# Performance work log

Hardware: AMD Instinct MI355X
Metric: run time of the kernel (lower is better)

Reference implementation:

```python
import jax, jax.numpy as jnp
import numpy as np

B, IN, H, OUT, T = 8192, 7, 256, 3, 200  # batch, input feats, hidden, output, seq_length


def setup_inputs() -> dict:
    key = jax.random.key(0)
    ks = iter(jax.random.split(key, 32))

    def W(shape, fan_in):
        return jax.random.normal(next(ks), shape, dtype=jnp.float32) * np.float32(1.0 / np.sqrt(fan_in))

    inp = {
        "x": jax.random.normal(next(ks), (B, IN), dtype=jnp.float32),
        # encoder: Linear(7,256) ReLU Linear(256,256) ReLU Linear(256,256) ReLU
        "enc_w1": W((H, IN), IN), "enc_b1": jnp.zeros((H,), jnp.float32),
        "enc_w2": W((H, H), H), "enc_b2": jnp.zeros((H,), jnp.float32),
        "enc_w3": W((H, H), H), "enc_b3": jnp.zeros((H,), jnp.float32),
        # hidden/cell init: Linear(256, 256*2)
        "hinit_w": W((2 * H, H), H), "hinit_b": jnp.zeros((2 * H,), jnp.float32),
        "cinit_w": W((2 * H, H), H), "cinit_b": jnp.zeros((2 * H,), jnp.float32),
        # LSTM layer 0 (input=3) and layer 1 (input=256); PyTorch gate order i,f,g,o
        "w_ih0": W((4 * H, OUT), H), "w_hh0": W((4 * H, H), H),
        "b_ih0": jnp.zeros((4 * H,), jnp.float32), "b_hh0": jnp.zeros((4 * H,), jnp.float32),
        "w_ih1": W((4 * H, H), H), "w_hh1": W((4 * H, H), H),
        "b_ih1": jnp.zeros((4 * H,), jnp.float32), "b_hh1": jnp.zeros((4 * H,), jnp.float32),
        # output head: Linear(256,128) ReLU Linear(128,3)
        "out_w1": W((H // 2, H), H), "out_b1": jnp.zeros((H // 2,), jnp.float32),
        "out_w2": W((OUT, H // 2), H // 2), "out_b2": jnp.zeros((OUT,), jnp.float32),
        "start_token": jnp.zeros((OUT,), jnp.float32),
    }
    return inp


def _lstm_cell(inp, h, c, w_ih, w_hh, b_ih, b_hh):
    gates = inp @ w_ih.T + b_ih + h @ w_hh.T + b_hh  # [B, 4H]
    i, f, g, o = jnp.split(gates, 4, axis=-1)
    c_new = jax.nn.sigmoid(f) * c + jax.nn.sigmoid(i) * jnp.tanh(g)
    h_new = jax.nn.sigmoid(o) * jnp.tanh(c_new)
    return h_new, c_new


def reference(x, enc_w1, enc_b1, enc_w2, enc_b2, enc_w3, enc_b3,
              hinit_w, hinit_b, cinit_w, cinit_b,
              w_ih0, w_hh0, b_ih0, b_hh0, w_ih1, w_hh1, b_ih1, b_hh1,
              out_w1, out_b1, out_w2, out_b2, start_token):
    b = x.shape[0]
    # MLP encoder (dropout inactive at inference)
    e = jax.nn.relu(x @ enc_w1.T + enc_b1)
    e = jax.nn.relu(e @ enc_w2.T + enc_b2)
    e = jax.nn.relu(e @ enc_w3.T + enc_b3)
    h0_all = (e @ hinit_w.T + hinit_b).reshape(b, 2, H)  # (batch, layers, H)
    c0_all = (e @ cinit_w.T + cinit_b).reshape(b, 2, H)
    h0, h1 = h0_all[:, 0], h0_all[:, 1]
    c0, c1 = c0_all[:, 0], c0_all[:, 1]
    dec = jnp.broadcast_to(start_token[None, :], (b, OUT))

    def step(carry, _):
        dec, h0, c0, h1, c1 = carry
        h0n, c0n = _lstm_cell(dec, h0, c0, w_ih0, w_hh0, b_ih0, b_hh0)
        h1n, c1n = _lstm_cell(h0n, h1, c1, w_ih1, w_hh1, b_ih1, b_hh1)
        out = jax.nn.relu(h1n @ out_w1.T + out_b1) @ out_w2.T + out_b2  # [B, 3]
        return (out, h0n, c0n, h1n, c1n), out

    _, outs = jax.lax.scan(step, (dec, h0, c0, h1, c1), None, length=T)
    return jnp.transpose(outs, (1, 0, 2))  # (batch, T, 3)
```

## Files before the change

### kernel.cpp

```cpp
#include <hip/hip_runtime.h>

typedef _Float16 f16;
typedef f16 h8v __attribute__((ext_vector_type(8)));
typedef f16 h4v __attribute__((ext_vector_type(4)));
typedef float f4v __attribute__((ext_vector_type(4)));

#define TT 200
#define NTHR 512
#define NWG 256

#define W0F   0
#define W1IF  262144
#define W1HF  524288
#define OW1F  786432
#define EW2F  819200
#define EW3F  884736
#define HIWF  950272
#define CIWF  1081344
#define FRAG_TOTAL 1212416
#define H0F   1212416
#define H1F   5406720
#define O1F   9601024
#define DECF  10649600
#define FLGF  10780672

#define FE1 0
#define FE2 1
#define FE3 2
#define FDEC 3
#define FH0 4
#define FH1 5
#define FO1 6

static __device__ __forceinline__ f4v mfma16(h8v a, h8v b, f4v c) {
  return __builtin_amdgcn_mfma_f32_16x16x32_f16(a, b, c, 0, 0, 0);
}
static __device__ __forceinline__ f4v fzero() { f4v z; z[0]=0.f; z[1]=0.f; z[2]=0.f; z[3]=0.f; return z; }
static __device__ __forceinline__ float rcpf(float x) { return __builtin_amdgcn_rcpf(x); }
static __device__ __forceinline__ float sigm(float x) { return rcpf(1.0f + __expf(-x)); }
static __device__ __forceinline__ float tanh2(float x) { return 1.0f - 2.0f * rcpf(1.0f + __expf(2.0f * x)); }

__global__ void conv_w(const float* __restrict__ whh0, const float* __restrict__ wih1,
                       const float* __restrict__ whh1, const float* __restrict__ ow1,
                       const float* __restrict__ ew2,  const float* __restrict__ ew3,
                       const float* __restrict__ hiw,  const float* __restrict__ ciw,
                       f16* __restrict__ dst, int* __restrict__ flags) {
  int i = blockIdx.x * 256 + threadIdx.x;
  if (blockIdx.x == 0 && threadIdx.x < 128) flags[threadIdx.x] = 0;
  if (i >= FRAG_TOTAL) return;
  const float* src; int base;
  if      (i < 262144)  { src = whh0; base = 0; }
  else if (i < 524288)  { src = wih1; base = 262144; }
  else if (i < 786432)  { src = whh1; base = 524288; }
  else if (i < 819200)  { src = ow1;  base = 786432; }
  else if (i < 884736)  { src = ew2;  base = 819200; }
  else if (i < 950272)  { src = ew3;  base = 884736; }
  else if (i < 1081344) { src = hiw;  base = 950272; }
  else                  { src = ciw;  base = 1081344; }
  int e = i - base;
  int row = e >> 8, col = e & 255;
  int idx = base + ((((row >> 4) << 5) + (col >> 3)) << 7) + ((row & 15) << 3) + (col & 7);
  dst[idx] = (f16)src[e];
}

#define RELF(fi)                                                               \
  do { __syncthreads();                                                        \
       if (tid == 0) __hip_atomic_fetch_add(&flg[fi], 1, __ATOMIC_RELAXED,     \
                                            __HIP_MEMORY_SCOPE_SYSTEM);        \
  } while (0)
#define WAITF(fi, tgt)                                                         \
  do { if (tid == 0) {                                                         \
         while (__hip_atomic_load(&flg[fi], __ATOMIC_RELAXED,                  \
                                  __HIP_MEMORY_SCOPE_SYSTEM) < (tgt))          \
           __builtin_amdgcn_s_sleep(2);                                        \
         (void)__hip_atomic_load(&flg[fi], __ATOMIC_ACQUIRE,                   \
                                 __HIP_MEMORY_SCOPE_SYSTEM);                   \
       }                                                                       \
       __syncthreads();                                                        \
  } while (0)

__global__ __launch_bounds__(NTHR, 1)
void traj_kernel(const float* __restrict__ x,
                 const float* __restrict__ ew1, const float* __restrict__ eb1,
                 const float* __restrict__ eb2, const float* __restrict__ eb3,
                 const float* __restrict__ hib, const float* __restrict__ cib,
                 const float* __restrict__ wih0,
                 const float* __restrict__ bih0, const float* __restrict__ bhh0,
                 const float* __restrict__ bih1, const float* __restrict__ bhh1,
                 const float* __restrict__ ob1, const float* __restrict__ ow2,
                 const float* __restrict__ ob2, const float* __restrict__ stok,
                 f16* __restrict__ ws, int* __restrict__ flags,
                 float* __restrict__ out)
{
  __shared__ __align__(16) f16 WL[13 * 4096];
  __shared__ __align__(16) float decsL[512 * 4];
  __shared__ __align__(16) f16 o1s[32 * 136];
  __shared__ float w2s[384];
  __shared__ float b0L[64];
  __shared__ float b1L[64];
  __shared__ float wiL[192];
  __shared__ float ob2s[4];

  const int tid  = threadIdx.x;
  const int bid  = blockIdx.x;
  const int g    = (bid & 7) + ((bid >> 7) << 3);
  const int m    = (bid >> 3) & 15;
  const int wv   = tid >> 6;
  const int lane = tid & 63;
  const int lr   = lane & 15;
  const int lg   = lane >> 4;

  int* flg = flags + g * 8;
  const int dcol = 16 * m + lr;

  f16* e1g = ws + H0F + g * 131072;
  f16* e2g = ws + H1F + g * 131072;
  f16* e3g = ws + H0F + (16 + g) * 131072;
  f16* o1g = ws + O1F + g * 65536;
  float* decb = (float*)(ws + DECF) + g * 4096;

  if (tid < 64) {
    const int G = tid >> 4, l = tid & 15;
    const int gc = G * 256 + 16 * m + l;
    b0L[tid] = bih0[gc] + bhh0[gc];
    b1L[tid] = bih1[gc] + bhh1[gc];
    wiL[tid * 3 + 0] = wih0[gc * 3 + 0];
    wiL[tid * 3 + 1] = wih0[gc * 3 + 1];
    wiL[tid * 3 + 2] = wih0[gc * 3 + 2];
  }
  const float ob1r = ob1[((m & 7) << 4) + lr];
  if (tid < 384) w2s[tid] = ow2[tid];
  if (tid < 3)   ob2s[tid] = ob2[tid];

  auto cptile = [&](int slot, int srcF) {
    ((h8v*)(WL + slot * 4096))[tid] = *(const h8v*)(ws + srcF + tid * 8);
  };
  auto BF = [&](int slot, int k) -> h8v {
    return ((const h8v*)WL)[slot * 512 + ((k << 2) + lg) * 16 + lr];
  };
  auto loadA8 = [&](const f16* gb, int R0, h8v* a) {
    const f16* p0 = gb + (lg >> 1) * 8192 + (size_t)(R0 + lr) * 16 + (lg & 1) * 8;
#pragma unroll
    for (int k = 0; k < 8; ++k) a[k] = *(const h8v*)(p0 + k * 16384);
  };

  cptile(0, EW2F + m * 4096);
  cptile(1, EW3F + m * 4096);
  cptile(2, HIWF + m * 4096);
  cptile(3, HIWF + (16 + m) * 4096);
  cptile(4, CIWF + m * 4096);
  cptile(5, CIWF + (16 + m) * 4096);
  __syncthreads();

  {
    const int r = tid;
    float xr[7];
#pragma unroll
    for (int k = 0; k < 7; ++k) xr[k] = x[(size_t)(g * 512 + r) * 7 + k];
    f16 ev[16];
#pragma unroll
    for (int i2 = 0; i2 < 16; ++i2) {
      const int c = 16 * m + i2;
      float a = eb1[c];
#pragma unroll
      for (int k = 0; k < 7; ++k) a += xr[k] * ew1[c * 7 + k];
      ev[i2] = (f16)fmaxf(a, 0.0f);
    }
    *(h8v*)(e1g + m * 8192 + r * 16)     = *(h8v*)&ev[0];
    *(h8v*)(e1g + m * 8192 + r * 16 + 8) = *(h8v*)&ev[8];
  }
  RELF(FE1); WAITF(FE1, 16);

  {
    const float bb = eb2[dcol];
#pragma unroll
    for (int mt = 0; mt < 4; ++mt) {
      const int R0 = wv * 64 + mt * 16;
      h8v a[8]; loadA8(e1g, R0, a);
      f4v acc = fzero();
#pragma unroll
      for (int k = 0; k < 8; ++k) acc = mfma16(a[k], BF(0, k), acc);
#pragma unroll
      for (int j = 0; j < 4; ++j)
        e2g[m * 8192 + (R0 + 4 * lg + j) * 16 + lr] = (f16)fmaxf(acc[j] + bb, 0.0f);
    }
  }
  RELF(FE2); WAITF(FE2, 16);

  {
    const float bb = eb3[dcol];
#pragma unroll
    for (int mt = 0; mt < 4; ++mt) {
      const int R0 = wv * 64 + mt * 16;
      h8v a[8]; loadA8(e2g, R0, a);
      f4v acc = fzero();
#pragma unroll
      for (int k = 0; k < 8; ++k) acc = mfma16(a[k], BF(1, k), acc);
#pragma unroll
      for (int j = 0; j < 4; ++j)
        e3g[m * 8192 + (R0 + 4 * lg + j) * 16 + lr] = (f16)fmaxf(acc[j] + bb, 0.0f);
    }
  }
  RELF(FE3); WAITF(FE3, 16);

  float c0v[4][4], c1v[4][4];
  {
    f16* h0g0 = ws + H0F + g * 131072;
    f16* h1g0 = ws + H1F + g * 131072;
    const float bh0 = hib[dcol], bh1 = hib[256 + dcol];
    const float bc0 = cib[dcol], bc1 = cib[256 + dcol];
#pragma unroll
    for (int mt = 0; mt < 4; ++mt) {
      const int R0 = wv * 64 + mt * 16;
      h8v a[8]; loadA8(e3g, R0, a);
      f4v aH = fzero(), aC = fzero();
#pragma unroll
      for (int k = 0; k < 8; ++k) { aH = mfma16(a[k], BF(2, k), aH); aC = mfma16(a[k], BF(4, k), aC); }
#pragma unroll
      for (int j = 0; j < 4; ++j) {
        h0g0[m * 8192 + (R0 + 4 * lg + j) * 16 + lr] = (f16)(aH[j] + bh0);
        c0v[mt][j] = aC[j] + bc0;
      }
      aH = fzero(); aC = fzero();
#pragma unroll
      for (int k = 0; k < 8; ++k) { aH = mfma16(a[k], BF(3, k), aH); aC = mfma16(a[k], BF(5, k), aC); }
#pragma unroll
      for (int j = 0; j < 4; ++j) {
        h1g0[m * 8192 + (R0 + 4 * lg + j) * 16 + lr] = (f16)(aH[j] + bh1);
        c1v[mt][j] = aC[j] + bc1;
      }
    }
    if (tid < 32) {
      f4v d; d[0] = stok[0]; d[1] = stok[1]; d[2] = stok[2]; d[3] = 0.f;
      *(f4v*)(decb + (m * 32 + tid) * 4) = d;
    }
  }
  RELF(FDEC);

#pragma unroll
  for (int G = 0; G < 4; ++G) {
    cptile(G,     W0F  + (G * 16 + m) * 4096);
    cptile(4 + G, W1IF + (G * 16 + m) * 4096);
    cptile(8 + G, W1HF + (G * 16 + m) * 4096);
  }
  cptile(12, OW1F + (m & 7) * 4096);
  __syncthreads();

  f4v g0a[4][4];
  WAITF(FDEC, 16);
  {
    const f16* h0old0 = ws + H0F + g * 131072;
#pragma unroll
    for (int mt = 0; mt < 4; ++mt) {
      const int R0 = wv * 64 + mt * 16;
      h8v a[8]; loadA8(h0old0, R0, a);
#pragma unroll
      for (int G = 0; G < 4; ++G) g0a[mt][G] = fzero();
#pragma unroll
      for (int k = 0; k < 8; ++k) {
        g0a[mt][0] = mfma16(a[k], BF(0, k), g0a[mt][0]);
        g0a[mt][1] = mfma16(a[k], BF(1, k), g0a[mt][1]);
        g0a[mt][2] = mfma16(a[k], BF(2, k), g0a[mt][2]);
        g0a[mt][3] = mfma16(a[k], BF(3, k), g0a[mt][3]);
      }
    }
  }

#pragma unroll 1
  for (int t = 0; t < TT; ++t) {
    const int p = t & 1;
    f16* h0new = ws + H0F + ((p ^ 1) * 16 + g) * 131072;
    f16* h1old = ws + H1F + (p * 16 + g) * 131072;
    f16* h1new = ws + H1F + ((p ^ 1) * 16 + g) * 131072;
    const float* decp = decb + p * 2048;
    float* decn = decb + (p ^ 1) * 2048;

    WAITF(FDEC, 16 * (t + 1));
    *(f4v*)(decsL + tid * 4) = *(const f4v*)(decp + tid * 4);
    __syncthreads();

    {
      float cb0[4], cw[4][3];
#pragma unroll
      for (int G = 0; G < 4; ++G) {
        cb0[G]   = b0L[G * 16 + lr];
        cw[G][0] = wiL[(G * 16 + lr) * 3 + 0];
        cw[G][1] = wiL[(G * 16 + lr) * 3 + 1];
        cw[G][2] = wiL[(G * 16 + lr) * 3 + 2];
      }
#pragma unroll
      for (int mt = 0; mt < 4; ++mt) {
        const int R0 = wv * 64 + mt * 16;
#pragma unroll
        for (int j = 0; j < 4; ++j) {
          const int row = R0 + 4 * lg + j;
          f4v d4 = *(const f4v*)(decsL + row * 4);
          float gi = g0a[mt][0][j] + cb0[0] + d4[0]*cw[0][0] + d4[1]*cw[0][1] + d4[2]*cw[0][2];
          float gf = g0a[mt][1][j] + cb0[1] + d4[0]*cw[1][0] + d4[1]*cw[1][1] + d4[2]*cw[1][2];
          float gg = g0a[mt][2][j] + cb0[2] + d4[0]*cw[2][0] + d4[1]*cw[2][1] + d4[2]*cw[2][2];
          float go = g0a[mt][3][j] + cb0[3] + d4[0]*cw[3][0] + d4[1]*cw[3][1] + d4[2]*cw[3][2];
          float cn = sigm(gf) * c0v[mt][j] + sigm(gi) * tanh2(gg);
          c0v[mt][j] = cn;
          h0new[m * 8192 + row * 16 + lr] = (f16)(sigm(go) * tanh2(cn));
        }
      }
    }
    RELF(FH0);

    f4v ph[2][4];
#pragma unroll
    for (int mt = 0; mt < 2; ++mt) {
      const int R0 = wv * 64 + mt * 16;
      h8v a[8]; loadA8(h1old, R0, a);
#pragma unroll
      for (int G = 0; G < 4; ++G) ph[mt][G] = fzero();
#pragma unroll
      for (int k = 0; k < 8; ++k) {
        ph[mt][0] = mfma16(a[k], BF(8,  k), ph[mt][0]);
        ph[mt][1] = mfma16(a[k], BF(9,  k), ph[mt][1]);
        ph[mt][2] = mfma16(a[k], BF(10, k), ph[mt][2]);
        ph[mt][3] = mfma16(a[k], BF(11, k), ph[mt][3]);
      }
    }
    WAITF(FH0, 16 * (t + 1));

    {
      float cb1[4];
#pragma unroll
      for (int G = 0; G < 4; ++G) cb1[G] = b1L[G * 16 + lr];
#pragma unroll
      for (int mt = 0; mt < 2; ++mt) {
        const int R0 = wv * 64 + mt * 16;
        h8v a[8]; loadA8(h0new, R0, a);
#pragma unroll
        for (int k = 0; k < 8; ++k) {
          ph[mt][0] = mfma16(a[k], BF(4, k), ph[mt][0]);
          ph[mt][1] = mfma16(a[k], BF(5, k), ph[mt][1]);
          ph[mt][2] = mfma16(a[k], BF(6, k), ph[mt][2]);
          ph[mt][3] = mfma16(a[k], BF(7, k), ph[mt][3]);
        }
#pragma unroll
        for (int j = 0; j < 4; ++j) {
          const int row = R0 + 4 * lg + j;
          float cn = sigm(ph[mt][1][j] + cb1[1]) * c1v[mt][j]
                   + sigm(ph[mt][0][j] + cb1[0]) * tanh2(ph[mt][2][j] + cb1[2]);
          c1v[mt][j] = cn;
          h1new[m * 8192 + row * 16 + lr] = (f16)(sigm(ph[mt][3][j] + cb1[3]) * tanh2(cn));
        }
      }
#pragma unroll
      for (int mt = 2; mt < 4; ++mt) {
        const int R0 = wv * 64 + mt * 16;
        f4v ai = fzero(), af = fzero(), ag = fzero(), ao = fzero();
        {
          h8v a[8]; loadA8(h1old, R0, a);
#pragma unroll
          for (int k = 0; k < 8; ++k) {
            ai = mfma16(a[k], BF(8,  k), ai);
            af = mfma16(a[k], BF(9,  k), af);
            ag = mfma16(a[k], BF(10, k), ag);
            ao = mfma16(a[k], BF(11, k), ao);
          }
        }
        {
          h8v a[8]; loadA8(h0new, R0, a);
#pragma unroll
          for (int k = 0; k < 8; ++k) {
            ai = mfma16(a[k], BF(4, k), ai);
            af = mfma16(a[k], BF(5, k), af);
            ag = mfma16(a[k], BF(6, k), ag);
            ao = mfma16(a[k], BF(7, k), ao);
          }
        }
#pragma unroll
        for (int j = 0; j < 4; ++j) {
          const int row = R0 + 4 * lg + j;
          float cn = sigm(af[j] + cb1[1]) * c1v[mt][j]
                   + sigm(ai[j] + cb1[0]) * tanh2(ag[j] + cb1[2]);
          c1v[mt][j] = cn;
          h1new[m * 8192 + row * 16 + lr] = (f16)(sigm(ao[j] + cb1[3]) * tanh2(cn));
        }
      }
    }
    RELF(FH1);

#pragma unroll
    for (int mt = 0; mt < 2; ++mt) {
      const int R0 = wv * 64 + mt * 16;
      h8v a[8]; loadA8(h0new, R0, a);
#pragma unroll
      for (int G = 0; G < 4; ++G) g0a[mt][G] = fzero();
#pragma unroll
      for (int k = 0; k < 8; ++k) {
        g0a[mt][0] = mfma16(a[k], BF(0, k), g0a[mt][0]);
        g0a[mt][1] = mfma16(a[k], BF(1, k), g0a[mt][1]);
        g0a[mt][2] = mfma16(a[k], BF(2, k), g0a[mt][2]);
        g0a[mt][3] = mfma16(a[k], BF(3, k), g0a[mt][3]);
      }
    }
    WAITF(FH1, 16 * (t + 1));

    {
      const int Rh = ((m >> 3) << 8) + wv * 32;
#pragma unroll
      for (int mt2 = 0; mt2 < 2; ++mt2) {
        const int R0 = Rh + mt2 * 16;
        h8v a[8]; loadA8(h1new, R0, a);
        f4v acc = fzero();
#pragma unroll
        for (int k = 0; k < 8; ++k) acc = mfma16(a[k], BF(12, k), acc);
#pragma unroll
        for (int j = 0; j < 4; ++j)
          o1g[(m & 7) * 8192 + (R0 + 4 * lg + j) * 16 + lr] =
              (f16)fmaxf(acc[j] + ob1r, 0.0f);
      }
    }
    RELF(FO1);

    {
      const int R0 = wv * 64 + 2 * 16;
      h8v a[8]; loadA8(h0new, R0, a);
#pragma unroll
      for (int G = 0; G < 4; ++G) g0a[2][G] = fzero();
#pragma unroll
      for (int k = 0; k < 8; ++k) {
        g0a[2][0] = mfma16(a[k], BF(0, k), g0a[2][0]);
        g0a[2][1] = mfma16(a[k], BF(1, k), g0a[2][1]);
        g0a[2][2] = mfma16(a[k], BF(2, k), g0a[2][2]);
        g0a[2][3] = mfma16(a[k], BF(3, k), g0a[2][3]);
      }
    }
    WAITF(FO1, 16 * (t + 1));

    {
      const int r32 = tid >> 4, t8 = (tid & 15) >> 1, hf = tid & 1;
      *(h8v*)(o1s + r32 * 136 + t8 * 16 + hf * 8) =
          *(const h8v*)(o1g + t8 * 8192 + (m * 32 + r32) * 16 + hf * 8);
    }
    __syncthreads();
    {
      const int r = tid >> 4, jj = tid & 15;
      float a0 = 0.f, a1 = 0.f, a2 = 0.f;
#pragma unroll
      for (int kk = 0; kk < 8; ++kk) {
        const int k = jj * 8 + kk;
        const float ov = (float)o1s[r * 136 + k];
        a0 += ov * w2s[k];
        a1 += ov * w2s[128 + k];
        a2 += ov * w2s[256 + k];
      }
#pragma unroll
      for (int s = 8; s >= 1; s >>= 1) {
        a0 += __shfl_xor(a0, s);
        a1 += __shfl_xor(a1, s);
        a2 += __shfl_xor(a2, s);
      }
      if (jj == 0) {
        a0 += ob2s[0]; a1 += ob2s[1]; a2 += ob2s[2];
        float* op = out + ((size_t)(g * 512 + m * 32 + r) * TT + t) * 3;
        op[0] = a0; op[1] = a1; op[2] = a2;
        f4v d; d[0] = a0; d[1] = a1; d[2] = a2; d[3] = 0.f;
        *(f4v*)(decn + (m * 32 + r) * 4) = d;
      }
    }
    RELF(FDEC);

    {
      const int R0 = wv * 64 + 3 * 16;
      h8v a[8]; loadA8(h0new, R0, a);
#pragma unroll
      for (int G = 0; G < 4; ++G) g0a[3][G] = fzero();
#pragma unroll
      for (int k = 0; k < 8; ++k) {
        g0a[3][0] = mfma16(a[k], BF(0, k), g0a[3][0]);
        g0a[3][1] = mfma16(a[k], BF(1, k), g0a[3][1]);
        g0a[3][2] = mfma16(a[k], BF(2, k), g0a[3][2]);
        g0a[3][3] = mfma16(a[k], BF(3, k), g0a[3][3]);
      }
    }
  }
}

extern "C" void kernel_launch(void* const* d_in, const int* in_sizes, int n_in,
                              void* d_out, int out_size, void* d_ws, size_t ws_size,
                              hipStream_t stream) {
  (void)in_sizes; (void)n_in; (void)out_size; (void)ws_size;
  f16* wk = (f16*)d_ws;
  int* flags = (int*)((char*)d_ws + (size_t)FLGF * 2);
  conv_w<<<(FRAG_TOTAL + 255) / 256, 256, 0, stream>>>(
      (const float*)d_in[12], (const float*)d_in[15],
      (const float*)d_in[16], (const float*)d_in[19],
      (const float*)d_in[3],  (const float*)d_in[5],
      (const float*)d_in[7],  (const float*)d_in[9],
      wk, flags);
  traj_kernel<<<NWG, NTHR, 0, stream>>>(
      (const float*)d_in[0],
      (const float*)d_in[1],  (const float*)d_in[2],
      (const float*)d_in[4],  (const float*)d_in[6],
      (const float*)d_in[8],  (const float*)d_in[10],
      (const float*)d_in[11],
      (const float*)d_in[13], (const float*)d_in[14],
      (const float*)d_in[17], (const float*)d_in[18],
      (const float*)d_in[20], (const float*)d_in[21],
      (const float*)d_in[22], (const float*)d_in[23],
      wk, flags, (float*)d_out);
}
```

Measured before the change: 5.214 ms.

## Compute output head redundantly per workgroup to drop decoder-token grid barrier

Each workgroup now computes the final 128->3 projection for all 512 rows of its group directly from global o1 data and writes the decoder token into its own shared memory. This removes the per-step FDEC cross-workgroup flag wait and the global round-trip for the decoder token, leaving one fewer grid-level synchronization per timestep. It also narrows atomic scopes from system to agent and shortens the spin sleep. In exchange every workgroup does 16x redundant head work and reads more global memory per step.

```diff
diff --git a/kernel.cpp b/kernel.cpp
--- a/kernel.cpp
+++ b/kernel.cpp
@@ -21,7 +21,6 @@
 #define H0F   1212416
 #define H1F   5406720
 #define O1F   9601024
-#define DECF  10649600
 #define FLGF  10780672
 
 #define FE1 0
@@ -66,15 +65,15 @@
 #define RELF(fi)                                                               \
   do { __syncthreads();                                                        \
        if (tid == 0) __hip_atomic_fetch_add(&flg[fi], 1, __ATOMIC_RELAXED,     \
-                                            __HIP_MEMORY_SCOPE_SYSTEM);        \
+                                            __HIP_MEMORY_SCOPE_AGENT);         \
   } while (0)
 #define WAITF(fi, tgt)                                                         \
   do { if (tid == 0) {                                                         \
          while (__hip_atomic_load(&flg[fi], __ATOMIC_RELAXED,                  \
-                                  __HIP_MEMORY_SCOPE_SYSTEM) < (tgt))          \
-           __builtin_amdgcn_s_sleep(2);                                        \
+                                  __HIP_MEMORY_SCOPE_AGENT) < (tgt))           \
+           __builtin_amdgcn_s_sleep(1);                                        \
          (void)__hip_atomic_load(&flg[fi], __ATOMIC_ACQUIRE,                   \
-                                 __HIP_MEMORY_SCOPE_SYSTEM);                   \
+                                 __HIP_MEMORY_SCOPE_AGENT);                    \
        }                                                                       \
        __syncthreads();                                                        \
   } while (0)
@@ -94,7 +93,6 @@
 {
   __shared__ __align__(16) f16 WL[13 * 4096];
   __shared__ __align__(16) float decsL[512 * 4];
-  __shared__ __align__(16) f16 o1s[32 * 136];
   __shared__ float w2s[384];
   __shared__ float b0L[64];
   __shared__ float b1L[64];
@@ -117,7 +115,6 @@
   f16* e2g = ws + H1F + g * 131072;
   f16* e3g = ws + H0F + (16 + g) * 131072;
   f16* o1g = ws + O1F + g * 65536;
-  float* decb = (float*)(ws + DECF) + g * 4096;
 
   if (tid < 64) {
     const int G = tid >> 4, l = tid & 15;
@@ -230,10 +227,6 @@
         c1v[mt][j] = aC[j] + bc1;
       }
     }
-    if (tid < 32) {
-      f4v d; d[0] = stok[0]; d[1] = stok[1]; d[2] = stok[2]; d[3] = 0.f;
-      *(f4v*)(decb + (m * 32 + tid) * 4) = d;
-    }
   }
   RELF(FDEC);
 
@@ -244,6 +237,11 @@
     cptile(8 + G, W1HF + (G * 16 + m) * 4096);
   }
   cptile(12, OW1F + (m & 7) * 4096);
+  {
+    const float s0 = stok[0], s1 = stok[1], s2 = stok[2];
+    decsL[tid * 4 + 0] = s0; decsL[tid * 4 + 1] = s1;
+    decsL[tid * 4 + 2] = s2; decsL[tid * 4 + 3] = 0.f;
+  }
   __syncthreads();
 
   f4v g0a[4][4];
@@ -272,12 +270,6 @@
     f16* h0new = ws + H0F + ((p ^ 1) * 16 + g) * 131072;
     f16* h1old = ws + H1F + (p * 16 + g) * 131072;
     f16* h1new = ws + H1F + ((p ^ 1) * 16 + g) * 131072;
-    const float* decp = decb + p * 2048;
-    float* decn = decb + (p ^ 1) * 2048;
-
-    WAITF(FDEC, 16 * (t + 1));
-    *(f4v*)(decsL + tid * 4) = *(const f4v*)(decp + tid * 4);
-    __syncthreads();
 
     {
       float cb0[4], cw[4][3];
@@ -417,67 +409,46 @@
     }
     RELF(FO1);
 
+#pragma unroll
+    for (int mt = 2; mt < 4; ++mt) {
+      const int R0 = wv * 64 + mt * 16;
+      h8v a[8]; loadA8(h0new, R0, a);
+#pragma unroll
+      for (int G = 0; G < 4; ++G) g0a[mt][G] = fzero();
+#pragma unroll
+      for (int k = 0; k < 8; ++k) {
+        g0a[mt][0] = mfma16(a[k], BF(0, k), g0a[mt][0]);
+        g0a[mt][1] = mfma16(a[k], BF(1, k), g0a[mt][1]);
+        g0a[mt][2] = mfma16(a[k], BF(2, k), g0a[mt][2]);
+        g0a[mt][3] = mfma16(a[k], BF(3, k), g0a[mt][3]);
+      }
+    }
+    WAITF(FO1, 16 * (t + 1));
+
     {
-      const int R0 = wv * 64 + 2 * 16;
-      h8v a[8]; loadA8(h0new, R0, a);
-#pragma unroll
-      for (int G = 0; G < 4; ++G) g0a[2][G] = fzero();
-#pragma unroll
-      for (int k = 0; k < 8; ++k) {
-        g0a[2][0] = mfma16(a[k], BF(0, k), g0a[2][0]);
-        g0a[2][1] = mfma16(a[k], BF(1, k), g0a[2][1]);
-        g0a[2][2] = mfma16(a[k], BF(2, k), g0a[2][2]);
-        g0a[2][3] = mfma16(a[k], BF(3, k), g0a[2][3]);
-      }
-    }
-    WAITF(FO1, 16 * (t + 1));
-
-    {
-      const int r32 = tid >> 4, t8 = (tid & 15) >> 1, hf = tid & 1;
-      *(h8v*)(o1s + r32 * 136 + t8 * 16 + hf * 8) =
-          *(const h8v*)(o1g + t8 * 8192 + (m * 32 + r32) * 16 + hf * 8);
+      const int r = tid;
+      float a0 = 0.f, a1 = 0.f, a2 = 0.f;
+#pragma unroll
+      for (int t8 = 0; t8 < 8; ++t8) {
+        h8v lo = *(const h8v*)(o1g + t8 * 8192 + r * 16);
+        h8v hi = *(const h8v*)(o1g + t8 * 8192 + r * 16 + 8);
+#pragma unroll
+        for (int j = 0; j < 8; ++j) {
+          const float v0 = (float)lo[j], v1 = (float)hi[j];
+          const int k0 = t8 * 16 + j, k1 = t8 * 16 + 8 + j;
+          a0 += v0 * w2s[k0]       + v1 * w2s[k1];
+          a1 += v0 * w2s[128 + k0] + v1 * w2s[128 + k1];
+          a2 += v0 * w2s[256 + k0] + v1 * w2s[256 + k1];
+        }
+      }
+      a0 += ob2s[0]; a1 += ob2s[1]; a2 += ob2s[2];
+      decsL[r * 4 + 0] = a0; decsL[r * 4 + 1] = a1; decsL[r * 4 + 2] = a2;
+      if ((tid >> 5) == m) {
+        float* op = out + ((size_t)(g * 512 + r) * TT + t) * 3;
+        op[0] = a0; op[1] = a1; op[2] = a2;
+      }
     }
     __syncthreads();
-    {
-      const int r = tid >> 4, jj = tid & 15;
-      float a0 = 0.f, a1 = 0.f, a2 = 0.f;
-#pragma unroll
-      for (int kk = 0; kk < 8; ++kk) {
-        const int k = jj * 8 + kk;
-        const float ov = (float)o1s[r * 136 + k];
-        a0 += ov * w2s[k];
-        a1 += ov * w2s[128 + k];
-        a2 += ov * w2s[256 + k];
-      }
-#pragma unroll
-      for (int s = 8; s >= 1; s >>= 1) {
-        a0 += __shfl_xor(a0, s);
-        a1 += __shfl_xor(a1, s);
-        a2 += __shfl_xor(a2, s);
-      }
-      if (jj == 0) {
-        a0 += ob2s[0]; a1 += ob2s[1]; a2 += ob2s[2];
-        float* op = out + ((size_t)(g * 512 + m * 32 + r) * TT + t) * 3;
-        op[0] = a0; op[1] = a1; op[2] = a2;
-        f4v d; d[0] = a0; d[1] = a1; d[2] = a2; d[3] = 0.f;
-        *(f4v*)(decn + (m * 32 + r) * 4) = d;
-      }
-    }
-    RELF(FDEC);
-
-    {
-      const int R0 = wv * 64 + 3 * 16;
-      h8v a[8]; loadA8(h0new, R0, a);
-#pragma unroll
-      for (int G = 0; G < 4; ++G) g0a[3][G] = fzero();
-#pragma unroll
-      for (int k = 0; k < 8; ++k) {
-        g0a[3][0] = mfma16(a[k], BF(0, k), g0a[3][0]);
-        g0a[3][1] = mfma16(a[k], BF(1, k), g0a[3][1]);
-        g0a[3][2] = mfma16(a[k], BF(2, k), g0a[3][2]);
-        g0a[3][3] = mfma16(a[k], BF(3, k), g0a[3][3]);
-      }
-    }
   }
 }
 
```

After: 6.094 ms. 1.17x slower.

## Compute output-head layer locally per block, drop FO1 cross-block barrier

Applied to the files above, without the earlier changes.

Each workgroup now computes the full 128-wide out_w1 hidden layer for its own 32 rows, reading the weight fragments directly from global memory. The result goes into fp32 LDS instead of being written to a global buffer and synchronised across 16 blocks through the FO1 flag. This removes one inter-workgroup barrier per timestep, at the cost of redundant out_w1 work per block and weight reads from global/L2 instead of LDS. Flag atomics also switch from system scope to agent scope, and the spin-wait sleep is shortened to cut synchronisation latency.

```diff
diff --git a/kernel.cpp b/kernel.cpp
--- a/kernel.cpp
+++ b/kernel.cpp
@@ -20,8 +20,7 @@
 #define FRAG_TOTAL 1212416
 #define H0F   1212416
 #define H1F   5406720
-#define O1F   9601024
-#define DECF  10649600
+#define DECF  9601024
 #define FLGF  10780672
 
 #define FE1 0
@@ -30,7 +29,6 @@
 #define FDEC 3
 #define FH0 4
 #define FH1 5
-#define FO1 6
 
 static __device__ __forceinline__ f4v mfma16(h8v a, h8v b, f4v c) {
   return __builtin_amdgcn_mfma_f32_16x16x32_f16(a, b, c, 0, 0, 0);
@@ -66,15 +64,15 @@
 #define RELF(fi)                                                               \
   do { __syncthreads();                                                        \
        if (tid == 0) __hip_atomic_fetch_add(&flg[fi], 1, __ATOMIC_RELAXED,     \
-                                            __HIP_MEMORY_SCOPE_SYSTEM);        \
+                                            __HIP_MEMORY_SCOPE_AGENT);         \
   } while (0)
 #define WAITF(fi, tgt)                                                         \
   do { if (tid == 0) {                                                         \
          while (__hip_atomic_load(&flg[fi], __ATOMIC_RELAXED,                  \
-                                  __HIP_MEMORY_SCOPE_SYSTEM) < (tgt))          \
-           __builtin_amdgcn_s_sleep(2);                                        \
+                                  __HIP_MEMORY_SCOPE_AGENT) < (tgt))           \
+           __builtin_amdgcn_s_sleep(1);                                        \
          (void)__hip_atomic_load(&flg[fi], __ATOMIC_ACQUIRE,                   \
-                                 __HIP_MEMORY_SCOPE_SYSTEM);                   \
+                                 __HIP_MEMORY_SCOPE_AGENT);                    \
        }                                                                       \
        __syncthreads();                                                        \
   } while (0)
@@ -92,10 +90,11 @@
                  f16* __restrict__ ws, int* __restrict__ flags,
                  float* __restrict__ out)
 {
-  __shared__ __align__(16) f16 WL[13 * 4096];
+  __shared__ __align__(16) f16 WL[12 * 4096];
   __shared__ __align__(16) float decsL[512 * 4];
-  __shared__ __align__(16) f16 o1s[32 * 136];
+  __shared__ __align__(16) float o1s[32 * 132];
   __shared__ float w2s[384];
+  __shared__ float ob1L[128];
   __shared__ float b0L[64];
   __shared__ float b1L[64];
   __shared__ float wiL[192];
@@ -116,7 +115,6 @@
   f16* e1g = ws + H0F + g * 131072;
   f16* e2g = ws + H1F + g * 131072;
   f16* e3g = ws + H0F + (16 + g) * 131072;
-  f16* o1g = ws + O1F + g * 65536;
   float* decb = (float*)(ws + DECF) + g * 4096;
 
   if (tid < 64) {
@@ -128,8 +126,8 @@
     wiL[tid * 3 + 1] = wih0[gc * 3 + 1];
     wiL[tid * 3 + 2] = wih0[gc * 3 + 2];
   }
-  const float ob1r = ob1[((m & 7) << 4) + lr];
   if (tid < 384) w2s[tid] = ow2[tid];
+  if (tid < 128) ob1L[tid] = ob1[tid];
   if (tid < 3)   ob2s[tid] = ob2[tid];
 
   auto cptile = [&](int slot, int srcF) {
@@ -243,7 +241,6 @@
     cptile(4 + G, W1IF + (G * 16 + m) * 4096);
     cptile(8 + G, W1HF + (G * 16 + m) * 4096);
   }
-  cptile(12, OW1F + (m & 7) * 4096);
   __syncthreads();
 
   f4v g0a[4][4];
@@ -401,21 +398,20 @@
     WAITF(FH1, 16 * (t + 1));
 
     {
-      const int Rh = ((m >> 3) << 8) + wv * 32;
-#pragma unroll
-      for (int mt2 = 0; mt2 < 2; ++mt2) {
-        const int R0 = Rh + mt2 * 16;
-        h8v a[8]; loadA8(h1new, R0, a);
-        f4v acc = fzero();
-#pragma unroll
-        for (int k = 0; k < 8; ++k) acc = mfma16(a[k], BF(12, k), acc);
+      const h8v* OW1G = (const h8v*)(ws + OW1F);
+#pragma unroll
+      for (int mt = 0; mt < 2; ++mt) {
+        h8v a[8]; loadA8(h1new, m * 32 + mt * 16, a);
+        f4v oacc = fzero();
+#pragma unroll
+        for (int k = 0; k < 8; ++k)
+          oacc = mfma16(a[k], OW1G[(wv << 9) + (((k << 2) + lg) << 4) + lr], oacc);
+        const float bo = ob1L[(wv << 4) + lr];
 #pragma unroll
         for (int j = 0; j < 4; ++j)
-          o1g[(m & 7) * 8192 + (R0 + 4 * lg + j) * 16 + lr] =
-              (f16)fmaxf(acc[j] + ob1r, 0.0f);
-      }
-    }
-    RELF(FO1);
+          o1s[(mt * 16 + 4 * lg + j) * 132 + (wv << 4) + lr] = fmaxf(oacc[j] + bo, 0.0f);
+      }
+    }
 
     {
       const int R0 = wv * 64 + 2 * 16;
@@ -430,21 +426,15 @@
         g0a[2][3] = mfma16(a[k], BF(3, k), g0a[2][3]);
       }
     }
-    WAITF(FO1, 16 * (t + 1));
-
-    {
-      const int r32 = tid >> 4, t8 = (tid & 15) >> 1, hf = tid & 1;
-      *(h8v*)(o1s + r32 * 136 + t8 * 16 + hf * 8) =
-          *(const h8v*)(o1g + t8 * 8192 + (m * 32 + r32) * 16 + hf * 8);
-    }
     __syncthreads();
+
     {
       const int r = tid >> 4, jj = tid & 15;
       float a0 = 0.f, a1 = 0.f, a2 = 0.f;
 #pragma unroll
       for (int kk = 0; kk < 8; ++kk) {
         const int k = jj * 8 + kk;
-        const float ov = (float)o1s[r * 136 + k];
+        const float ov = o1s[r * 132 + k];
         a0 += ov * w2s[k];
         a1 += ov * w2s[128 + k];
         a2 += ov * w2s[256 + k];
@@ -457,10 +447,11 @@
       }
       if (jj == 0) {
         a0 += ob2s[0]; a1 += ob2s[1]; a2 += ob2s[2];
-        float* op = out + ((size_t)(g * 512 + m * 32 + r) * TT + t) * 3;
+        const int row = m * 32 + r;
+        float* op = out + ((size_t)(g * 512 + row) * TT + t) * 3;
         op[0] = a0; op[1] = a1; op[2] = a2;
         f4v d; d[0] = a0; d[1] = a1; d[2] = a2; d[3] = 0.f;
-        *(f4v*)(decn + (m * 32 + r) * 4) = d;
+        *(f4v*)(decn + row * 4) = d;
       }
     }
     RELF(FDEC);
```

After: 4.707 ms. -9.7%, faster.
